# Optimization experiments

Measured on AMD Instinct MI355X. Metric: run time of the kernel, lower is better.

## Reference

```python
import jax, jax.numpy as jnp
import numpy as np

B_, S_, P_, D_ = 2, 512, 64, 1024
L_ = 4            # n_layer
DI_ = 2 * D_      # d_inner (expand=2)
DS_ = 16          # d_state
DC_ = 4           # d_conv
DR_ = D_ // 16    # dt_rank
PCD_ = 768        # prepend_cond_dim


def setup_inputs() -> dict:
    key = jax.random.key(0)
    ks = jax.random.split(key, 12)
    n = lambda k, s, sc=0.02: jax.random.normal(k, s, dtype=jnp.float32) * sc
    A_log = jnp.log(jnp.broadcast_to(jnp.arange(1, DS_ + 1, dtype=jnp.float32), (L_, DI_, DS_)))
    return {
        'x': jax.random.normal(ks[0], (B_, S_, D_), dtype=jnp.float32),
        'prepend_cond': jax.random.normal(ks[1], (B_, P_, PCD_), dtype=jnp.float32),
        'pre_w1': n(ks[2], (PCD_, D_)),
        'pre_w2': n(ks[3], (D_, D_)),
        'norm_w': jnp.ones((L_, D_), jnp.float32),
        'in_proj_w': n(ks[4], (L_, 2 * DI_, D_)),
        'conv_w': n(ks[5], (L_, DI_, DC_), 0.1),
        'conv_b': jnp.zeros((L_, DI_), jnp.float32),
        'x_proj_w': n(ks[6], (L_, DR_ + 2 * DS_, DI_)),
        'dt_proj_w': n(ks[7], (L_, DI_, DR_), 0.1),
        'dt_proj_b': jax.random.uniform(ks[8], (L_, DI_), jnp.float32, -4.0, -2.0),
        'A_log': A_log,
        'D_param': jnp.ones((L_, DI_), jnp.float32),
        'out_proj_w': n(ks[9], (L_, D_, DI_)),
        'final_norm_w': jnp.ones((D_,), jnp.float32),
    }


def rmsnorm(x, w, eps=1e-5):
    return x * jax.lax.rsqrt(jnp.mean(x * x, axis=-1, keepdims=True) + eps) * w


def mamba_block(x, ip_w, cw, cb, xp_w, dtp_w, dtp_b, A_log, Dp, op_w):
    B, S, _ = x.shape
    xz = jnp.einsum('bsd,ed->bse', x, ip_w)            # [B,S,2*DI]
    xi, z = jnp.split(xz, 2, axis=-1)
    # depthwise causal conv1d along time
    xt = xi.transpose(0, 2, 1)                          # [B,DI,S]
    conv = jax.lax.conv_general_dilated(
        xt, cw[:, None, :], (1,), [(DC_ - 1, 0)], feature_group_count=DI_) + cb[:, None]
    xi = jax.nn.silu(conv.transpose(0, 2, 1))           # [B,S,DI]
    xdbl = jnp.einsum('bse,fe->bsf', xi, xp_w)          # [B,S,DR+2*DS]
    dt, Bm, Cm = jnp.split(xdbl, [DR_, DR_ + DS_], axis=-1)
    dt = jax.nn.softplus(jnp.einsum('bsr,er->bse', dt, dtp_w) + dtp_b)  # [B,S,DI]
    A = -jnp.exp(A_log)                                 # [DI,DS]
    dA = jnp.exp(dt[..., None] * A)                     # [B,S,DI,DS]
    dBu = dt[..., None] * Bm[:, :, None, :] * xi[..., None]

    def step(h, t):
        da, dbu, c = t
        h = da * h + dbu                                # [B,DI,DS]
        return h, jnp.einsum('bes,bs->be', h, c)

    h0 = jnp.zeros((B, DI_, DS_), x.dtype)
    _, ys = jax.lax.scan(step, h0, (dA.transpose(1, 0, 2, 3), dBu.transpose(1, 0, 2, 3), Cm.transpose(1, 0, 2)))
    y = ys.transpose(1, 0, 2) + xi * Dp
    y = y * jax.nn.silu(z)
    return jnp.einsum('bse,de->bsd', y, op_w)


def reference(x, prepend_cond, pre_w1, pre_w2, norm_w, in_proj_w, conv_w, conv_b,
              x_proj_w, dt_proj_w, dt_proj_b, A_log, D_param, out_proj_w, final_norm_w):
    p = jax.nn.silu(prepend_cond @ pre_w1) @ pre_w2     # to_prepend_embed
    h = jnp.concatenate([p, x], axis=1)                 # [B, P+S, D]
    for l in range(L_):
        h = h + mamba_block(rmsnorm(h, norm_w[l]), in_proj_w[l], conv_w[l], conv_b[l],
                            x_proj_w[l], dt_proj_w[l], dt_proj_b[l], A_log[l],
                            D_param[l], out_proj_w[l])
    h = rmsnorm(h, final_norm_w)
    return h[:, P_:, :]
```

## Files before the change

kernel.cpp:

```cpp
#include <hip/hip_runtime.h>
#include <math.h>

#define B_ 2
#define S_ 512
#define P_ 64
#define T_ 576
#define D_ 1024
#define L_ 4
#define DI_ 2048
#define DS_ 16
#define DC_ 4
#define DR_ 64
#define PCD_ 768
#define M_ (B_*T_)
#define CCH 18
#define NC (T_/CCH)
#define XKS 16
#define OPK 4

typedef __attribute__((ext_vector_type(8))) short bf16x8;
typedef __attribute__((ext_vector_type(4))) float f32x4;

__device__ __forceinline__ float silu_f(float v) { return v / (1.f + __expf(-v)); }
__device__ __forceinline__ float softplus_f(float v) {
    return fmaxf(v, 0.f) + log1pf(__expf(-fabsf(v)));
}
__device__ __forceinline__ unsigned short bf16_rne(float x) {
    unsigned int b = __float_as_uint(x);
    b += 0x7fffu + ((b >> 16) & 1u);
    return (unsigned short)(b >> 16);
}
__device__ __forceinline__ float bf16_to_f(unsigned short u) {
    return __uint_as_float((unsigned int)u << 16);
}

typedef const void __attribute__((address_space(1)))* gas_t;
typedef void __attribute__((address_space(3)))* las_t;
__device__ __forceinline__ void async16(const void* g, void* l) {
    __builtin_amdgcn_global_load_lds((gas_t)g, (las_t)l, 16, 0, 0);
}

template<int EPI, int BN>
__global__ __launch_bounds__(256) void gemm_mfma_kernel(
    const unsigned short* __restrict__ A, const unsigned short* __restrict__ W,
    float* __restrict__ C, float* __restrict__ C2,
    int M, int N, int K, int Kchunk)
{
    constexpr int NF = BN / 32;
    __shared__ unsigned short As[128 * 32];
    __shared__ unsigned short Bs[BN * 32];
    const int tid = threadIdx.x;
    const int wave = tid >> 6;
    const int lane = tid & 63;
    const int m0 = blockIdx.y * 128, n0 = blockIdx.x * BN;
    const int kbase = blockIdx.z * Kchunk;
    const int wm = (wave >> 1) * 64, wn = (wave & 1) * (BN / 2);

    const int srow = (wave << 5) + (lane >> 2);
    const int selem = (lane & 3) * 8;
    const unsigned short* gA = A + (size_t)(m0 + srow) * K + kbase + selem;
    const unsigned short* gB = W + (size_t)(n0 + srow) * K + kbase + selem;
    unsigned short* lA = As + (wave << 5) * 32;
    unsigned short* lB = Bs + (wave << 5) * 32;

    f32x4 acc[4][NF];
    #pragma unroll
    for (int i = 0; i < 4; ++i)
        #pragma unroll
        for (int j = 0; j < NF; ++j)
            acc[i][j] = (f32x4){0.f, 0.f, 0.f, 0.f};

    const int fr = lane & 15;
    const int fq = lane >> 4;
    const int aoff = (wm + fr) * 32 + fq * 8;
    const int boff = (wn + fr) * 32 + fq * 8;

    for (int k0 = 0; k0 < Kchunk; k0 += 32) {
        async16(gA, lA);
        async16(gA + (size_t)16 * K, lA + 16 * 32);
        if (BN == 128 || wave < BN / 32) {
            async16(gB, lB);
            async16(gB + (size_t)16 * K, lB + 16 * 32);
        }
        gA += 32; gB += 32;
        __syncthreads();
        bf16x8 af[4], bf[NF];
        #pragma unroll
        for (int i = 0; i < 4; ++i) af[i] = *(const bf16x8*)&As[aoff + i * 512];
        #pragma unroll
        for (int j = 0; j < NF; ++j) bf[j] = *(const bf16x8*)&Bs[boff + j * 512];
        #pragma unroll
        for (int i = 0; i < 4; ++i)
            #pragma unroll
            for (int j = 0; j < NF; ++j)
                acc[i][j] = __builtin_amdgcn_mfma_f32_16x16x32_bf16(
                    af[i], bf[j], acc[i][j], 0, 0, 0);
        __syncthreads();
    }

    #pragma unroll
    for (int i = 0; i < 4; ++i) {
        const int m = m0 + wm + i * 16 + fq * 4;
        #pragma unroll
        for (int j = 0; j < NF; ++j) {
            const int n = n0 + wn + j * 16 + fr;
            if (EPI == 6) {
                float* p = C + ((size_t)blockIdx.z * M + m) * N + n;
                #pragma unroll
                for (int r = 0; r < 4; ++r)
                    p[(size_t)r * N] = acc[i][j][r];
            } else if (EPI == 7) {
                if (n < DI_) {
                    unsigned short* p = (unsigned short*)C + (size_t)m * DI_ + n;
                    #pragma unroll
                    for (int r = 0; r < 4; ++r)
                        p[(size_t)r * DI_] = bf16_rne(acc[i][j][r]);
                } else {
                    unsigned short* p = (unsigned short*)C2 + (size_t)m * DI_ + (n - DI_);
                    #pragma unroll
                    for (int r = 0; r < 4; ++r)
                        p[(size_t)r * DI_] = bf16_rne(silu_f(acc[i][j][r]));
                }
            }
        }
    }
}

__global__ __launch_bounds__(256) void dtproj_kernel(
    const unsigned short* __restrict__ dtr,
    const unsigned short* __restrict__ Wb,
    const float* __restrict__ bias,
    float* __restrict__ dtb)
{
    __shared__ float As[16][DR_];
    const int tid = threadIdx.x;
    const int e = blockIdx.x * 256 + tid;
    const int m0 = blockIdx.y * 16;
    {
        const ushort4 a4 = ((const ushort4*)(dtr + (size_t)m0 * DR_))[tid];
        float* dst = &As[0][0] + tid * 4;
        dst[0] = bf16_to_f(a4.x);
        dst[1] = bf16_to_f(a4.y);
        dst[2] = bf16_to_f(a4.z);
        dst[3] = bf16_to_f(a4.w);
    }
    float w[DR_];
    {
        const ushort4* wp = (const ushort4*)(Wb + (size_t)e * DR_);
        #pragma unroll
        for (int q = 0; q < 16; ++q) {
            const ushort4 v = wp[q];
            w[q * 4 + 0] = bf16_to_f(v.x);
            w[q * 4 + 1] = bf16_to_f(v.y);
            w[q * 4 + 2] = bf16_to_f(v.z);
            w[q * 4 + 3] = bf16_to_f(v.w);
        }
    }
    __syncthreads();
    const float bb = bias[e];
    #pragma unroll
    for (int m = 0; m < 16; ++m) {
        float acc = 0.f;
        #pragma unroll
        for (int r = 0; r < DR_; ++r) acc = fmaf(As[m][r], w[r], acc);
        dtb[(size_t)(m0 + m) * DI_ + e] = softplus_f(acc + bb);
    }
}

__global__ __launch_bounds__(256) void xproj_mfma_kernel(
    const unsigned short* __restrict__ A,
    const unsigned short* __restrict__ W,
    float* __restrict__ P)
{
    __shared__ unsigned short As[128 * 32];
    __shared__ unsigned short Bs[96 * 32];
    const int tid = threadIdx.x;
    const int wave = tid >> 6;
    const int lane = tid & 63;
    const int m0 = blockIdx.y * 128;
    const int kbase = blockIdx.x * (DI_ / XKS);
    const int wm = (wave >> 1) * 64, wn = (wave & 1) * 48;

    const int srow = (wave << 5) + (lane >> 2);
    const int selem = (lane & 3) * 8;
    const unsigned short* gA = A + (size_t)(m0 + srow) * DI_ + kbase + selem;
    const unsigned short* gB = W + (size_t)srow * DI_ + kbase + selem;
    unsigned short* lA = As + (wave << 5) * 32;
    unsigned short* lB = Bs + (wave << 5) * 32;

    f32x4 acc[4][3];
    #pragma unroll
    for (int i = 0; i < 4; ++i)
        #pragma unroll
        for (int j = 0; j < 3; ++j)
            acc[i][j] = (f32x4){0.f, 0.f, 0.f, 0.f};

    const int fr = lane & 15;
    const int fq = lane >> 4;
    const int aoff = (wm + fr) * 32 + fq * 8;
    const int boff = (wn + fr) * 32 + fq * 8;

    #pragma unroll
    for (int kk = 0; kk < 4; ++kk) {
        async16(gA, lA);
        async16(gA + (size_t)16 * DI_, lA + 16 * 32);
        if (wave < 3) {
            async16(gB, lB);
            async16(gB + (size_t)16 * DI_, lB + 16 * 32);
        }
        gA += 32; gB += 32;
        __syncthreads();
        bf16x8 af[4], bf[3];
        #pragma unroll
        for (int i = 0; i < 4; ++i) af[i] = *(const bf16x8*)&As[aoff + i * 512];
        #pragma unroll
        for (int j = 0; j < 3; ++j) bf[j] = *(const bf16x8*)&Bs[boff + j * 512];
        #pragma unroll
        for (int i = 0; i < 4; ++i)
            #pragma unroll
            for (int j = 0; j < 3; ++j)
                acc[i][j] = __builtin_amdgcn_mfma_f32_16x16x32_bf16(
                    af[i], bf[j], acc[i][j], 0, 0, 0);
        __syncthreads();
    }

    float* Pb = P + ((size_t)blockIdx.x * M_ + m0) * 96;
    #pragma unroll
    for (int i = 0; i < 4; ++i) {
        const int m = wm + i * 16 + fq * 4;
        #pragma unroll
        for (int j = 0; j < 3; ++j) {
            const int n = wn + j * 16 + fr;
            #pragma unroll
            for (int r = 0; r < 4; ++r)
                Pb[(size_t)(m + r) * 96 + n] = acc[i][j][r];
        }
    }
}

__global__ __launch_bounds__(256) void xproj_reduce_kernel(
    const float* __restrict__ P, float* __restrict__ Bc, float* __restrict__ Cc,
    unsigned short* __restrict__ dtr_bf)
{
    const int i = blockIdx.x * 256 + threadIdx.x;
    if (i >= M_ * 96) return;
    float s = 0.f;
    #pragma unroll
    for (int ks = 0; ks < XKS; ++ks) s += P[(size_t)ks * (M_ * 96) + i];
    const int m = i / 96;
    const int n = i - m * 96;
    if (n < DR_)            dtr_bf[(size_t)m * DR_ + n] = bf16_rne(s);
    else if (n < DR_ + DS_) Bc[(size_t)m * DS_ + (n - DR_)] = s;
    else                    Cc[(size_t)m * DS_ + (n - DR_ - DS_)] = s;
}

__global__ __launch_bounds__(256) void cvt_bf16_kernel(
    const float* __restrict__ in, unsigned short* __restrict__ out, int n4)
{
    const int i = blockIdx.x * 256 + threadIdx.x;
    if (i >= n4) return;
    const float4 v = ((const float4*)in)[i];
    ushort4 o;
    o.x = bf16_rne(v.x); o.y = bf16_rne(v.y);
    o.z = bf16_rne(v.z); o.w = bf16_rne(v.w);
    ((ushort4*)out)[i] = o;
}

__global__ __launch_bounds__(256) void cvt4_kernel(
    const float* __restrict__ s0, unsigned short* __restrict__ d0, int n0,
    const float* __restrict__ s1, unsigned short* __restrict__ d1, int n1,
    const float* __restrict__ s2, unsigned short* __restrict__ d2, int n2,
    const float* __restrict__ s3, unsigned short* __restrict__ d3, int n3)
{
    const int i = blockIdx.x * 256 + threadIdx.x;
    const float* s; unsigned short* d; int off;
    if (i < n0)                { s = s0; d = d0; off = i; }
    else if (i < n0 + n1)      { s = s1; d = d1; off = i - n0; }
    else if (i < n0 + n1 + n2) { s = s2; d = d2; off = i - n0 - n1; }
    else if (i < n0 + n1 + n2 + n3) { s = s3; d = d3; off = i - n0 - n1 - n2; }
    else return;
    const float4 v = ((const float4*)s)[off];
    ushort4 o;
    o.x = bf16_rne(v.x); o.y = bf16_rne(v.y);
    o.z = bf16_rne(v.z); o.w = bf16_rne(v.w);
    ((ushort4*)d)[off] = o;
}

__global__ __launch_bounds__(256) void cvt_transpose_kernel(
    const float* __restrict__ in, unsigned short* __restrict__ out, int K, int N)
{
    __shared__ float t[64][65];
    const int k0 = blockIdx.x * 64;
    const int n0 = blockIdx.y * 64;
    const int tx = threadIdx.x & 63;
    const int ty = threadIdx.x >> 6;
    #pragma unroll
    for (int j = 0; j < 16; ++j) {
        const int kk = ty * 16 + j;
        t[kk][tx] = in[(size_t)(k0 + kk) * N + n0 + tx];
    }
    __syncthreads();
    #pragma unroll
    for (int j = 0; j < 16; ++j) {
        const int nn = ty * 16 + j;
        out[(size_t)(n0 + nn) * K + k0 + tx] = bf16_rne(t[tx][nn]);
    }
}

__global__ __launch_bounds__(256) void reduce_silu_bf16_kernel(
    const float* __restrict__ P, unsigned short* __restrict__ o, int MN, int ns)
{
    const int i = blockIdx.x * 256 + threadIdx.x;
    if (i >= MN) return;
    float s = 0.f;
    for (int k = 0; k < ns; ++k) s += P[(size_t)k * MN + i];
    o[i] = bf16_rne(silu_f(s));
}
__global__ __launch_bounds__(256) void reduce_fp32_kernel(
    const float* __restrict__ P, float* __restrict__ o, int MN, int ns)
{
    const int i = blockIdx.x * 256 + threadIdx.x;
    if (i >= MN) return;
    float s = 0.f;
    for (int k = 0; k < ns; ++k) s += P[(size_t)k * MN + i];
    o[i] = s;
}

__global__ __launch_bounds__(256) void outproj_rmsnorm_kernel(
    const float* __restrict__ P, float* __restrict__ h,
    const float* __restrict__ w, unsigned short* __restrict__ outb, int donorm)
{
    const int r = blockIdx.x;
    const int i = r * 256 + threadIdx.x;
    float4 v = ((float4*)h)[i];
    #pragma unroll
    for (int k = 0; k < OPK; ++k) {
        const float4 a4 = ((const float4*)P)[i + k * (M_ * D_ / 4)];
        v.x += a4.x; v.y += a4.y; v.z += a4.z; v.w += a4.w;
    }
    ((float4*)h)[i] = v;
    if (!donorm) return;
    float ss = v.x * v.x + v.y * v.y + v.z * v.z + v.w * v.w;
    ss += __shfl_xor(ss, 32, 64);
    ss += __shfl_xor(ss, 16, 64);
    ss += __shfl_xor(ss, 8, 64);
    ss += __shfl_xor(ss, 4, 64);
    ss += __shfl_xor(ss, 2, 64);
    ss += __shfl_xor(ss, 1, 64);
    __shared__ float red[4];
    if ((threadIdx.x & 63) == 0) red[threadIdx.x >> 6] = ss;
    __syncthreads();
    const float tot = red[0] + red[1] + red[2] + red[3];
    const float scale = rsqrtf(tot * (1.f / D_) + 1e-5f);
    const float4 wv = ((const float4*)w)[threadIdx.x];
    ushort4 o;
    o.x = bf16_rne(v.x * scale * wv.x);
    o.y = bf16_rne(v.y * scale * wv.y);
    o.z = bf16_rne(v.z * scale * wv.z);
    o.w = bf16_rne(v.w * scale * wv.w);
    ((ushort4*)(outb + (size_t)r * D_))[threadIdx.x] = o;
}

__global__ __launch_bounds__(256) void assemble_h_kernel(
    const float* __restrict__ p, const float* __restrict__ x, float* __restrict__ h)
{
    const int idx = blockIdx.x * 256 + threadIdx.x;
    const int r = idx >> 8;
    const int c = idx & 255;
    const int b = r / T_;
    const int t = r - b * T_;
    float4 v;
    if (t < P_) v = ((const float4*)p)[(size_t)(b * P_ + t) * 256 + c];
    else        v = ((const float4*)x)[(size_t)(b * S_ + (t - P_)) * 256 + c];
    ((float4*)h)[idx] = v;
}

__global__ __launch_bounds__(256) void rmsnorm_bf16_kernel(
    const float* __restrict__ x, const float* __restrict__ w,
    unsigned short* __restrict__ outb)
{
    const int r = blockIdx.x;
    const float4 v = ((const float4*)(x + (size_t)r * D_))[threadIdx.x];
    float ss = v.x * v.x + v.y * v.y + v.z * v.z + v.w * v.w;
    ss += __shfl_xor(ss, 32, 64);
    ss += __shfl_xor(ss, 16, 64);
    ss += __shfl_xor(ss, 8, 64);
    ss += __shfl_xor(ss, 4, 64);
    ss += __shfl_xor(ss, 2, 64);
    ss += __shfl_xor(ss, 1, 64);
    __shared__ float red[4];
    if ((threadIdx.x & 63) == 0) red[threadIdx.x >> 6] = ss;
    __syncthreads();
    const float tot = red[0] + red[1] + red[2] + red[3];
    const float scale = rsqrtf(tot * (1.f / D_) + 1e-5f);
    const float4 wv = ((const float4*)w)[threadIdx.x];
    ushort4 o;
    o.x = bf16_rne(v.x * scale * wv.x);
    o.y = bf16_rne(v.y * scale * wv.y);
    o.z = bf16_rne(v.z * scale * wv.z);
    o.w = bf16_rne(v.w * scale * wv.w);
    ((ushort4*)(outb + (size_t)r * D_))[threadIdx.x] = o;
}

__global__ __launch_bounds__(256) void final_rmsnorm_kernel(
    const float* __restrict__ h, const float* __restrict__ w, float* __restrict__ out)
{
    const int r = blockIdx.x;
    const int b = r / S_;
    const int s = r - b * S_;
    const int hr = b * T_ + P_ + s;
    const float4 v = ((const float4*)(h + (size_t)hr * D_))[threadIdx.x];
    float ss = v.x * v.x + v.y * v.y + v.z * v.z + v.w * v.w;
    ss += __shfl_xor(ss, 32, 64);
    ss += __shfl_xor(ss, 16, 64);
    ss += __shfl_xor(ss, 8, 64);
    ss += __shfl_xor(ss, 4, 64);
    ss += __shfl_xor(ss, 2, 64);
    ss += __shfl_xor(ss, 1, 64);
    __shared__ float red[4];
    if ((threadIdx.x & 63) == 0) red[threadIdx.x >> 6] = ss;
    __syncthreads();
    const float tot = red[0] + red[1] + red[2] + red[3];
    const float scale = rsqrtf(tot * (1.f / D_) + 1e-5f);
    const float4 wv = ((const float4*)w)[threadIdx.x];
    float4 o;
    o.x = v.x * scale * wv.x; o.y = v.y * scale * wv.y;
    o.z = v.z * scale * wv.z; o.w = v.w * scale * wv.w;
    ((float4*)(out + (size_t)r * D_))[threadIdx.x] = o;
}

__global__ __launch_bounds__(256) void conv_silu_kernel(
    const unsigned short* __restrict__ xb, const float* __restrict__ cw,
    const float* __restrict__ cb, unsigned short* __restrict__ xib)
{
    __shared__ float xs[67][64];
    const int tid = threadIdx.x;
    const int tx = tid & 63;
    const int ty = tid >> 6;
    const int r0 = blockIdx.x * 64;
    const int e0 = blockIdx.y * 64;
    const int bt0 = (r0 / T_) * T_;

    for (int j = ty; j < 67; j += 4) {
        const int r = r0 + j - 3;
        xs[j][tx] = (r >= bt0) ? bf16_to_f(xb[(size_t)r * DI_ + e0 + tx]) : 0.f;
    }
    __syncthreads();
    const float4 w = *(const float4*)(cw + (size_t)(e0 + tx) * 4);
    const float bias = cb[e0 + tx];
    #pragma unroll
    for (int j = 0; j < 16; ++j) {
        const int rl = ty * 16 + j;
        float v = bias;
        v = fmaf(w.x, xs[rl + 0][tx], v);
        v = fmaf(w.y, xs[rl + 1][tx], v);
        v = fmaf(w.z, xs[rl + 2][tx], v);
        v = fmaf(w.w, xs[rl + 3][tx], v);
        xib[(size_t)(r0 + rl) * DI_ + e0 + tx] = bf16_rne(silu_f(v));
    }
}

__global__ __launch_bounds__(256) void scan_chunk1_kernel(
    const float* __restrict__ dtm,
    const float* __restrict__ Bc,
    const unsigned short* __restrict__ xib,
    const float* __restrict__ A_log,
    float* __restrict__ Ap, float* __restrict__ Hp)
{
    __shared__ float4 Bs[CCH][4];
    const int tid = threadIdx.x;
    const int e = ((blockIdx.x & 7) << 8) + tid;
    const int cb = blockIdx.x >> 3;
    const int b = cb & (B_ - 1);
    const int c = cb >> 1;
    const int r0 = b * T_ + c * CCH;
    for (int i = tid; i < CCH * DS_; i += 256)
        ((float*)Bs)[i] = Bc[(size_t)r0 * DS_ + i];
    float A2[DS_], h[DS_], a[DS_];
    const float* Ae = A_log + (size_t)e * DS_;
    #pragma unroll
    for (int s = 0; s < DS_; ++s) {
        A2[s] = -__expf(Ae[s]) * 1.44269504f;
        h[s] = 0.f; a[s] = 1.f;
    }
    __syncthreads();
    const float* dp = dtm + (size_t)r0 * DI_ + e;
    const unsigned short* up = xib + (size_t)r0 * DI_ + e;
    #pragma unroll
    for (int t = 0; t < CCH; ++t) {
        const float dtv = dp[(size_t)t * DI_];
        const float dtu = dtv * bf16_to_f(up[(size_t)t * DI_]);
        #pragma unroll
        for (int q = 0; q < 4; ++q) {
            const float4 bq = Bs[t][q];
            const float* bb = &bq.x;
            #pragma unroll
            for (int j = 0; j < 4; ++j) {
                const int s = q * 4 + j;
                const float da = __builtin_amdgcn_exp2f(dtv * A2[s]);
                a[s] *= da;
                h[s] = fmaf(da, h[s], bb[j] * dtu);
            }
        }
    }
    const size_t o = (size_t)cb * DS_ * DI_ + e;
    #pragma unroll
    for (int s = 0; s < DS_; ++s) {
        Ap[o + (size_t)s * DI_] = a[s];
        Hp[o + (size_t)s * DI_] = h[s];
    }
}

__global__ __launch_bounds__(256) void scan_chunk2_kernel(
    float* __restrict__ Ap, float* __restrict__ Hp)
{
    const int g = blockIdx.x * 256 + threadIdx.x;
    float h = 0.f;
    #pragma unroll
    for (int c = 0; c < NC; ++c) {
        const size_t o = (size_t)c * (B_ * DI_ * DS_) + g;
        const float ap = Ap[o];
        const float hp = Hp[o];
        Hp[o] = h;
        h = fmaf(ap, h, hp);
    }
}

__global__ __launch_bounds__(256) void scan_chunk3_kernel(
    const float* __restrict__ dtm,
    const float* __restrict__ Bc,
    const float* __restrict__ Cc,
    const unsigned short* __restrict__ xib,
    const unsigned short* __restrict__ szb,
    const float* __restrict__ A_log, const float* __restrict__ Dp,
    const float* __restrict__ Hin, unsigned short* __restrict__ y)
{
    __shared__ float4 Bs[CCH][4], Cs[CCH][4];
    const int tid = threadIdx.x;
    const int e = ((blockIdx.x & 7) << 8) + tid;
    const int cb = blockIdx.x >> 3;
    const int b = cb & (B_ - 1);
    const int c = cb >> 1;
    const int r0 = b * T_ + c * CCH;
    for (int i = tid; i < CCH * DS_; i += 256) {
        ((float*)Bs)[i] = Bc[(size_t)r0 * DS_ + i];
        ((float*)Cs)[i] = Cc[(size_t)r0 * DS_ + i];
    }
    float A2[DS_], h[DS_];
    const float* Ae = A_log + (size_t)e * DS_;
    const float dpe = Dp[e];
    const size_t ho = (size_t)cb * DS_ * DI_ + e;
    #pragma unroll
    for (int s = 0; s < DS_; ++s) {
        A2[s] = -__expf(Ae[s]) * 1.44269504f;
        h[s] = Hin[ho + (size_t)s * DI_];
    }
    __syncthreads();
    const float* dp = dtm + (size_t)r0 * DI_ + e;
    const unsigned short* up = xib + (size_t)r0 * DI_ + e;
    const unsigned short* sp = szb + (size_t)r0 * DI_ + e;
    unsigned short* yp = y + (size_t)r0 * DI_ + e;
    #pragma unroll
    for (int t = 0; t < CCH; ++t) {
        const float dtv = dp[(size_t)t * DI_];
        const float u   = bf16_to_f(up[(size_t)t * DI_]);
        const float dtu = dtv * u;
        float y0 = 0.f, y1 = 0.f, y2 = 0.f, y3 = 0.f;
        #pragma unroll
        for (int q = 0; q < 4; ++q) {
            const float4 bq = Bs[t][q];
            const float4 cq = Cs[t][q];
            const float* bb = &bq.x;
            const float* cc = &cq.x;
            #pragma unroll
            for (int j = 0; j < 4; ++j) {
                const int s = q * 4 + j;
                const float da = __builtin_amdgcn_exp2f(dtv * A2[s]);
                h[s] = fmaf(da, h[s], bb[j] * dtu);
                if (j == 0)      y0 = fmaf(h[s], cc[j], y0);
                else if (j == 1) y1 = fmaf(h[s], cc[j], y1);
                else if (j == 2) y2 = fmaf(h[s], cc[j], y2);
                else             y3 = fmaf(h[s], cc[j], y3);
            }
        }
        const float ysum = (y0 + y1) + (y2 + y3);
        const float yv = fmaf(u, dpe, ysum) * bf16_to_f(sp[(size_t)t * DI_]);
        yp[(size_t)t * DI_] = bf16_rne(yv);
    }
}

extern "C" void kernel_launch(void* const* d_in, const int* in_sizes, int n_in,
                              void* d_out, int out_size, void* d_ws, size_t ws_size,
                              hipStream_t stream)
{
    const float* x       = (const float*)d_in[0];
    const float* pc      = (const float*)d_in[1];
    const float* pre_w1  = (const float*)d_in[2];
    const float* pre_w2  = (const float*)d_in[3];
    const float* norm_w  = (const float*)d_in[4];
    const float* ip_w    = (const float*)d_in[5];
    const float* conv_w  = (const float*)d_in[6];
    const float* conv_b  = (const float*)d_in[7];
    const float* xp_w    = (const float*)d_in[8];
    const float* dtp_w   = (const float*)d_in[9];
    const float* dtp_b   = (const float*)d_in[10];
    const float* A_log   = (const float*)d_in[11];
    const float* D_param = (const float*)d_in[12];
    const float* op_w    = (const float*)d_in[13];
    const float* fnw     = (const float*)d_in[14];
    float* out = (float*)d_out;

    float* ws = (float*)d_ws;
    float* h    = ws;  ws += (size_t)M_ * D_;
    float* xz   = ws;  ws += (size_t)M_ * 2 * DI_;
    float* dtb  = ws;  ws += (size_t)M_ * DI_;
    float* Pbuf = ws;  ws += (size_t)XKS * M_ * 96;
    float* Bc   = ws;  ws += (size_t)DS_ * M_;
    float* Cc   = ws;  ws += (size_t)DS_ * M_;
    unsigned short* xn_bf  = (unsigned short*)ws;  ws += (size_t)M_ * D_ / 2;
    unsigned short* yb_bf  = (unsigned short*)ws;  ws += (size_t)M_ * DI_ / 2;
    unsigned short* xi_bf  = (unsigned short*)ws;  ws += (size_t)M_ * DI_ / 2;
    unsigned short* xb_bf  = (unsigned short*)ws;  ws += (size_t)M_ * DI_ / 2;
    unsigned short* szb_bf = (unsigned short*)ws;  ws += (size_t)M_ * DI_ / 2;
    unsigned short* dtr_bf = (unsigned short*)ws;  ws += (size_t)M_ * DR_ / 2;
    unsigned short* wbuf   = (unsigned short*)ws;  ws += (size_t)2 * DI_ * D_ / 2;
    unsigned short* xpw_bf = (unsigned short*)ws;  ws += (size_t)96 * DI_ / 2;
    unsigned short* dtpw_bf= (unsigned short*)ws;  ws += (size_t)DI_ * DR_ / 2;
    unsigned short* opw_bf = (unsigned short*)ws;  ws += (size_t)D_ * DI_ / 2;

    float* Ap = xz;
    float* Hp = xz + (size_t)NC * B_ * DI_ * DS_;

    unsigned short* pc_bf   = xi_bf;
    unsigned short* w1t_bf  = wbuf;
    unsigned short* w2t_bf  = wbuf + (size_t)D_ * PCD_;
    unsigned short* tmp1_bf = xn_bf;
    float*          tmp2    = Pbuf;
    float*          P2buf   = dtb;
    float*          Pop     = xz;

    const dim3 blk(256);

    cvt_bf16_kernel<<<dim3(B_ * P_ * PCD_ / 4 / 256), blk, 0, stream>>>(
        pc, pc_bf, B_ * P_ * PCD_ / 4);
    cvt_transpose_kernel<<<dim3(PCD_ / 64, D_ / 64), blk, 0, stream>>>(
        pre_w1, w1t_bf, PCD_, D_);
    cvt_transpose_kernel<<<dim3(D_ / 64, D_ / 64), blk, 0, stream>>>(
        pre_w2, w2t_bf, D_, D_);
    gemm_mfma_kernel<6, 64><<<dim3(D_ / 64, 1, 12), blk, 0, stream>>>(
        pc_bf, w1t_bf, Pbuf, nullptr, B_ * P_, D_, PCD_, PCD_ / 12);
    reduce_silu_bf16_kernel<<<dim3(B_ * P_ * D_ / 256), blk, 0, stream>>>(
        Pbuf, tmp1_bf, B_ * P_ * D_, 12);
    gemm_mfma_kernel<6, 64><<<dim3(D_ / 64, 1, 16), blk, 0, stream>>>(
        tmp1_bf, w2t_bf, P2buf, nullptr, B_ * P_, D_, D_, D_ / 16);
    reduce_fp32_kernel<<<dim3(B_ * P_ * D_ / 256), blk, 0, stream>>>(
        P2buf, tmp2, B_ * P_ * D_, 16);
    assemble_h_kernel<<<dim3(M_ * D_ / 4 / 256), blk, 0, stream>>>(tmp2, x, h);

    const int n_ip  = 2 * DI_ * D_ / 4;
    const int n_xp  = 96 * DI_ / 4;
    const int n_dtp = DI_ * DR_ / 4;
    const int n_op  = D_ * DI_ / 4;

    rmsnorm_bf16_kernel<<<dim3(M_), blk, 0, stream>>>(h, norm_w, xn_bf);

    for (int l = 0; l < L_; ++l) {
        cvt4_kernel<<<dim3((n_ip + n_xp + n_dtp + n_op + 255) / 256), blk, 0, stream>>>(
            ip_w + (size_t)l * 2 * DI_ * D_, wbuf, n_ip,
            xp_w + (size_t)l * 96 * DI_, xpw_bf, n_xp,
            dtp_w + (size_t)l * DI_ * DR_, dtpw_bf, n_dtp,
            op_w + (size_t)l * D_ * DI_, opw_bf, n_op);
        gemm_mfma_kernel<7, 64><<<dim3(2 * DI_ / 64, M_ / 128, 1), blk, 0, stream>>>(
            xn_bf, wbuf, (float*)xb_bf, (float*)szb_bf, M_, 2 * DI_, D_, D_);
        conv_silu_kernel<<<dim3(M_ / 64, DI_ / 64), blk, 0, stream>>>(
            xb_bf, conv_w + (size_t)l * DI_ * DC_, conv_b + (size_t)l * DI_,
            xi_bf);
        xproj_mfma_kernel<<<dim3(XKS, M_ / 128), blk, 0, stream>>>(
            xi_bf, xpw_bf, Pbuf);
        xproj_reduce_kernel<<<dim3((M_ * 96 + 255) / 256), blk, 0, stream>>>(
            Pbuf, Bc, Cc, dtr_bf);
        dtproj_kernel<<<dim3(DI_ / 256, M_ / 16), blk, 0, stream>>>(
            dtr_bf, dtpw_bf, dtp_b + (size_t)l * DI_, dtb);
        scan_chunk1_kernel<<<dim3(NC * B_ * DI_ / 256), blk, 0, stream>>>(
            dtb, Bc, xi_bf, A_log + (size_t)l * DI_ * DS_, Ap, Hp);
        scan_chunk2_kernel<<<dim3(B_ * DI_ * DS_ / 256), blk, 0, stream>>>(Ap, Hp);
        scan_chunk3_kernel<<<dim3(NC * B_ * DI_ / 256), blk, 0, stream>>>(
            dtb, Bc, Cc, xi_bf, szb_bf, A_log + (size_t)l * DI_ * DS_,
            D_param + (size_t)l * DI_, Hp, yb_bf);
        gemm_mfma_kernel<6, 64><<<dim3(D_ / 64, M_ / 128, OPK), blk, 0, stream>>>(
            yb_bf, opw_bf, Pop, nullptr, M_, D_, DI_, DI_ / OPK);
        outproj_rmsnorm_kernel<<<dim3(M_), blk, 0, stream>>>(
            Pop, h, norm_w + (size_t)((l + 1) & 3) * D_, xn_bf, l < L_ - 1);
    }

    final_rmsnorm_kernel<<<dim3(B_ * S_), blk, 0, stream>>>(h, fnw, out);
}
```

Before: 681.1 us.

## Fuse dt projection into scan kernels, double-buffer weight conversion, bf16 out-proj partials

Removes the standalone dtproj kernel and its fp32 dt buffer, recomputing dt (a 64-wide dot plus softplus) inside both scan_chunk1 and scan_chunk3 from dtr held in LDS. The per-layer weight conversion is folded into the rmsnorm and outproj-residual kernels as extra blocks that convert the next layer's weights into a second buffer set. Out-proj split-K partials are now stored as bf16 instead of fp32, halving that traffic at some precision cost. The dt projection is now computed twice per layer, and each scan thread must hold 64 weight values in registers.

```diff
diff --git a/kernel.cpp b/kernel.cpp
--- a/kernel.cpp
+++ b/kernel.cpp
@@ -18,6 +18,13 @@
 #define XKS 16
 #define OPK 4
 
+#define N_IP (2*DI_*D_/4)
+#define N_XP (96*DI_/4)
+#define N_DTP (DI_*DR_/4)
+#define N_OP (D_*DI_/4)
+#define CVB ((N_IP + N_XP + N_DTP + N_OP + 255) / 256)
+#define SETSZ ((size_t)2*DI_*D_ + 96*DI_ + DI_*DR_ + D_*DI_)
+
 typedef __attribute__((ext_vector_type(8))) short bf16x8;
 typedef __attribute__((ext_vector_type(4))) float f32x4;
 
@@ -38,6 +45,25 @@
 typedef void __attribute__((address_space(3)))* las_t;
 __device__ __forceinline__ void async16(const void* g, void* l) {
     __builtin_amdgcn_global_load_lds((gas_t)g, (las_t)l, 16, 0, 0);
+}
+
+__device__ __forceinline__ void cvt4_body(int i,
+    const float* s0, unsigned short* d0, int n0,
+    const float* s1, unsigned short* d1, int n1,
+    const float* s2, unsigned short* d2, int n2,
+    const float* s3, unsigned short* d3, int n3)
+{
+    const float* s; unsigned short* d; int off;
+    if (i < n0)                     { s = s0; d = d0; off = i; }
+    else if (i < n0 + n1)           { s = s1; d = d1; off = i - n0; }
+    else if (i < n0 + n1 + n2)      { s = s2; d = d2; off = i - n0 - n1; }
+    else if (i < n0 + n1 + n2 + n3) { s = s3; d = d3; off = i - n0 - n1 - n2; }
+    else return;
+    const float4 v = ((const float4*)s)[off];
+    ushort4 o;
+    o.x = bf16_rne(v.x); o.y = bf16_rne(v.y);
+    o.z = bf16_rne(v.z); o.w = bf16_rne(v.w);
+    ((ushort4*)d)[off] = o;
 }
 
 template<int EPI, int BN>
@@ -109,6 +135,12 @@
                 #pragma unroll
                 for (int r = 0; r < 4; ++r)
                     p[(size_t)r * N] = acc[i][j][r];
+            } else if (EPI == 8) {
+                unsigned short* p = (unsigned short*)C +
+                                    ((size_t)blockIdx.z * M + m) * N + n;
+                #pragma unroll
+                for (int r = 0; r < 4; ++r)
+                    p[(size_t)r * N] = bf16_rne(acc[i][j][r]);
             } else if (EPI == 7) {
                 if (n < DI_) {
                     unsigned short* p = (unsigned short*)C + (size_t)m * DI_ + n;
@@ -126,47 +158,6 @@
     }
 }
 
-__global__ __launch_bounds__(256) void dtproj_kernel(
-    const unsigned short* __restrict__ dtr,
-    const unsigned short* __restrict__ Wb,
-    const float* __restrict__ bias,
-    float* __restrict__ dtb)
-{
-    __shared__ float As[16][DR_];
-    const int tid = threadIdx.x;
-    const int e = blockIdx.x * 256 + tid;
-    const int m0 = blockIdx.y * 16;
-    {
-        const ushort4 a4 = ((const ushort4*)(dtr + (size_t)m0 * DR_))[tid];
-        float* dst = &As[0][0] + tid * 4;
-        dst[0] = bf16_to_f(a4.x);
-        dst[1] = bf16_to_f(a4.y);
-        dst[2] = bf16_to_f(a4.z);
-        dst[3] = bf16_to_f(a4.w);
-    }
-    float w[DR_];
-    {
-        const ushort4* wp = (const ushort4*)(Wb + (size_t)e * DR_);
-        #pragma unroll
-        for (int q = 0; q < 16; ++q) {
-            const ushort4 v = wp[q];
-            w[q * 4 + 0] = bf16_to_f(v.x);
-            w[q * 4 + 1] = bf16_to_f(v.y);
-            w[q * 4 + 2] = bf16_to_f(v.z);
-            w[q * 4 + 3] = bf16_to_f(v.w);
-        }
-    }
-    __syncthreads();
-    const float bb = bias[e];
-    #pragma unroll
-    for (int m = 0; m < 16; ++m) {
-        float acc = 0.f;
-        #pragma unroll
-        for (int r = 0; r < DR_; ++r) acc = fmaf(As[m][r], w[r], acc);
-        dtb[(size_t)(m0 + m) * DI_ + e] = softplus_f(acc + bb);
-    }
-}
-
 __global__ __launch_bounds__(256) void xproj_mfma_kernel(
     const unsigned short* __restrict__ A,
     const unsigned short* __restrict__ W,
@@ -266,26 +257,6 @@
     ((ushort4*)out)[i] = o;
 }
 
-__global__ __launch_bounds__(256) void cvt4_kernel(
-    const float* __restrict__ s0, unsigned short* __restrict__ d0, int n0,
-    const float* __restrict__ s1, unsigned short* __restrict__ d1, int n1,
-    const float* __restrict__ s2, unsigned short* __restrict__ d2, int n2,
-    const float* __restrict__ s3, unsigned short* __restrict__ d3, int n3)
-{
-    const int i = blockIdx.x * 256 + threadIdx.x;
-    const float* s; unsigned short* d; int off;
-    if (i < n0)                { s = s0; d = d0; off = i; }
-    else if (i < n0 + n1)      { s = s1; d = d1; off = i - n0; }
-    else if (i < n0 + n1 + n2) { s = s2; d = d2; off = i - n0 - n1; }
-    else if (i < n0 + n1 + n2 + n3) { s = s3; d = d3; off = i - n0 - n1 - n2; }
-    else return;
-    const float4 v = ((const float4*)s)[off];
-    ushort4 o;
-    o.x = bf16_rne(v.x); o.y = bf16_rne(v.y);
-    o.z = bf16_rne(v.z); o.w = bf16_rne(v.w);
-    ((ushort4*)d)[off] = o;
-}
-
 __global__ __launch_bounds__(256) void cvt_transpose_kernel(
     const float* __restrict__ in, unsigned short* __restrict__ out, int K, int N)
 {
@@ -326,17 +297,28 @@
     o[i] = s;
 }
 
-__global__ __launch_bounds__(256) void outproj_rmsnorm_kernel(
-    const float* __restrict__ P, float* __restrict__ h,
-    const float* __restrict__ w, unsigned short* __restrict__ outb, int donorm)
-{
-    const int r = blockIdx.x;
+__global__ __launch_bounds__(256) void outproj_rmsnorm_cvt_kernel(
+    const unsigned short* __restrict__ P, float* __restrict__ h,
+    const float* __restrict__ w, unsigned short* __restrict__ outb, int donorm,
+    const float* s0, unsigned short* d0, int n0,
+    const float* s1, unsigned short* d1, int n1,
+    const float* s2, unsigned short* d2, int n2,
+    const float* s3, unsigned short* d3, int n3)
+{
+    const int bid = blockIdx.x;
+    if (bid >= M_) {
+        cvt4_body((bid - M_) * 256 + threadIdx.x,
+                  s0, d0, n0, s1, d1, n1, s2, d2, n2, s3, d3, n3);
+        return;
+    }
+    const int r = bid;
     const int i = r * 256 + threadIdx.x;
     float4 v = ((float4*)h)[i];
     #pragma unroll
     for (int k = 0; k < OPK; ++k) {
-        const float4 a4 = ((const float4*)P)[i + k * (M_ * D_ / 4)];
-        v.x += a4.x; v.y += a4.y; v.z += a4.z; v.w += a4.w;
+        const ushort4 a4 = ((const ushort4*)P)[(size_t)k * (M_ * D_ / 4) + i];
+        v.x += bf16_to_f(a4.x); v.y += bf16_to_f(a4.y);
+        v.z += bf16_to_f(a4.z); v.w += bf16_to_f(a4.w);
     }
     ((float4*)h)[i] = v;
     if (!donorm) return;
@@ -375,11 +357,21 @@
     ((float4*)h)[idx] = v;
 }
 
-__global__ __launch_bounds__(256) void rmsnorm_bf16_kernel(
+__global__ __launch_bounds__(256) void rmsnorm_cvt_kernel(
     const float* __restrict__ x, const float* __restrict__ w,
-    unsigned short* __restrict__ outb)
-{
-    const int r = blockIdx.x;
+    unsigned short* __restrict__ outb,
+    const float* s0, unsigned short* d0, int n0,
+    const float* s1, unsigned short* d1, int n1,
+    const float* s2, unsigned short* d2, int n2,
+    const float* s3, unsigned short* d3, int n3)
+{
+    const int bid = blockIdx.x;
+    if (bid >= M_) {
+        cvt4_body((bid - M_) * 256 + threadIdx.x,
+                  s0, d0, n0, s1, d1, n1, s2, d2, n2, s3, d3, n3);
+        return;
+    }
+    const int r = bid;
     const float4 v = ((const float4*)(x + (size_t)r * D_))[threadIdx.x];
     float ss = v.x * v.x + v.y * v.y + v.z * v.z + v.w * v.w;
     ss += __shfl_xor(ss, 32, 64);
@@ -461,13 +453,16 @@
 }
 
 __global__ __launch_bounds__(256) void scan_chunk1_kernel(
-    const float* __restrict__ dtm,
+    const unsigned short* __restrict__ dtr,
+    const unsigned short* __restrict__ dtw,
+    const float* __restrict__ dtbias,
     const float* __restrict__ Bc,
     const unsigned short* __restrict__ xib,
     const float* __restrict__ A_log,
     float* __restrict__ Ap, float* __restrict__ Hp)
 {
     __shared__ float4 Bs[CCH][4];
+    __shared__ float dtrs[CCH][DR_];
     const int tid = threadIdx.x;
     const int e = ((blockIdx.x & 7) << 8) + tid;
     const int cb = blockIdx.x >> 3;
@@ -476,6 +471,12 @@
     const int r0 = b * T_ + c * CCH;
     for (int i = tid; i < CCH * DS_; i += 256)
         ((float*)Bs)[i] = Bc[(size_t)r0 * DS_ + i];
+    for (int i = tid; i < CCH * DR_ / 4; i += 256) {
+        const ushort4 v4 = ((const ushort4*)(dtr + (size_t)r0 * DR_))[i];
+        float* d = &dtrs[0][0] + i * 4;
+        d[0] = bf16_to_f(v4.x); d[1] = bf16_to_f(v4.y);
+        d[2] = bf16_to_f(v4.z); d[3] = bf16_to_f(v4.w);
+    }
     float A2[DS_], h[DS_], a[DS_];
     const float* Ae = A_log + (size_t)e * DS_;
     #pragma unroll
@@ -484,11 +485,31 @@
         h[s] = 0.f; a[s] = 1.f;
     }
     __syncthreads();
-    const float* dp = dtm + (size_t)r0 * DI_ + e;
+    float dt[CCH];
+    {
+        float w[DR_];
+        const ushort4* wp = (const ushort4*)(dtw + (size_t)e * DR_);
+        #pragma unroll
+        for (int q = 0; q < 16; ++q) {
+            const ushort4 v = wp[q];
+            w[q * 4 + 0] = bf16_to_f(v.x);
+            w[q * 4 + 1] = bf16_to_f(v.y);
+            w[q * 4 + 2] = bf16_to_f(v.z);
+            w[q * 4 + 3] = bf16_to_f(v.w);
+        }
+        const float bb = dtbias[e];
+        #pragma unroll
+        for (int t = 0; t < CCH; ++t) {
+            float acc = 0.f;
+            #pragma unroll
+            for (int r = 0; r < DR_; ++r) acc = fmaf(dtrs[t][r], w[r], acc);
+            dt[t] = softplus_f(acc + bb);
+        }
+    }
     const unsigned short* up = xib + (size_t)r0 * DI_ + e;
     #pragma unroll
     for (int t = 0; t < CCH; ++t) {
-        const float dtv = dp[(size_t)t * DI_];
+        const float dtv = dt[t];
         const float dtu = dtv * bf16_to_f(up[(size_t)t * DI_]);
         #pragma unroll
         for (int q = 0; q < 4; ++q) {
@@ -527,7 +548,9 @@
 }
 
 __global__ __launch_bounds__(256) void scan_chunk3_kernel(
-    const float* __restrict__ dtm,
+    const unsigned short* __restrict__ dtr,
+    const unsigned short* __restrict__ dtw,
+    const float* __restrict__ dtbias,
     const float* __restrict__ Bc,
     const float* __restrict__ Cc,
     const unsigned short* __restrict__ xib,
@@ -536,6 +559,7 @@
     const float* __restrict__ Hin, unsigned short* __restrict__ y)
 {
     __shared__ float4 Bs[CCH][4], Cs[CCH][4];
+    __shared__ float dtrs[CCH][DR_];
     const int tid = threadIdx.x;
     const int e = ((blockIdx.x & 7) << 8) + tid;
     const int cb = blockIdx.x >> 3;
@@ -546,6 +570,12 @@
         ((float*)Bs)[i] = Bc[(size_t)r0 * DS_ + i];
         ((float*)Cs)[i] = Cc[(size_t)r0 * DS_ + i];
     }
+    for (int i = tid; i < CCH * DR_ / 4; i += 256) {
+        const ushort4 v4 = ((const ushort4*)(dtr + (size_t)r0 * DR_))[i];
+        float* d = &dtrs[0][0] + i * 4;
+        d[0] = bf16_to_f(v4.x); d[1] = bf16_to_f(v4.y);
+        d[2] = bf16_to_f(v4.z); d[3] = bf16_to_f(v4.w);
+    }
     float A2[DS_], h[DS_];
     const float* Ae = A_log + (size_t)e * DS_;
     const float dpe = Dp[e];
@@ -556,13 +586,33 @@
         h[s] = Hin[ho + (size_t)s * DI_];
     }
     __syncthreads();
-    const float* dp = dtm + (size_t)r0 * DI_ + e;
+    float dt[CCH];
+    {
+        float w[DR_];
+        const ushort4* wp = (const ushort4*)(dtw + (size_t)e * DR_);
+        #pragma unroll
+        for (int q = 0; q < 16; ++q) {
+            const ushort4 v = wp[q];
+            w[q * 4 + 0] = bf16_to_f(v.x);
+            w[q * 4 + 1] = bf16_to_f(v.y);
+            w[q * 4 + 2] = bf16_to_f(v.z);
+            w[q * 4 + 3] = bf16_to_f(v.w);
+        }
+        const float bb = dtbias[e];
+        #pragma unroll
+        for (int t = 0; t < CCH; ++t) {
+            float acc = 0.f;
+            #pragma unroll
+            for (int r = 0; r < DR_; ++r) acc = fmaf(dtrs[t][r], w[r], acc);
+            dt[t] = softplus_f(acc + bb);
+        }
+    }
     const unsigned short* up = xib + (size_t)r0 * DI_ + e;
     const unsigned short* sp = szb + (size_t)r0 * DI_ + e;
     unsigned short* yp = y + (size_t)r0 * DI_ + e;
     #pragma unroll
     for (int t = 0; t < CCH; ++t) {
-        const float dtv = dp[(size_t)t * DI_];
+        const float dtv = dt[t];
         const float u   = bf16_to_f(up[(size_t)t * DI_]);
         const float dtu = dtv * u;
         float y0 = 0.f, y1 = 0.f, y2 = 0.f, y3 = 0.f;
@@ -613,7 +663,7 @@
     float* ws = (float*)d_ws;
     float* h    = ws;  ws += (size_t)M_ * D_;
     float* xz   = ws;  ws += (size_t)M_ * 2 * DI_;
-    float* dtb  = ws;  ws += (size_t)M_ * DI_;
+    float* scr  = ws;  ws += (size_t)M_ * DI_;
     float* Pbuf = ws;  ws += (size_t)XKS * M_ * 96;
     float* Bc   = ws;  ws += (size_t)DS_ * M_;
     float* Cc   = ws;  ws += (size_t)DS_ * M_;
@@ -623,21 +673,28 @@
     unsigned short* xb_bf  = (unsigned short*)ws;  ws += (size_t)M_ * DI_ / 2;
     unsigned short* szb_bf = (unsigned short*)ws;  ws += (size_t)M_ * DI_ / 2;
     unsigned short* dtr_bf = (unsigned short*)ws;  ws += (size_t)M_ * DR_ / 2;
-    unsigned short* wbuf   = (unsigned short*)ws;  ws += (size_t)2 * DI_ * D_ / 2;
-    unsigned short* xpw_bf = (unsigned short*)ws;  ws += (size_t)96 * DI_ / 2;
-    unsigned short* dtpw_bf= (unsigned short*)ws;  ws += (size_t)DI_ * DR_ / 2;
-    unsigned short* opw_bf = (unsigned short*)ws;  ws += (size_t)D_ * DI_ / 2;
+    unsigned short* wsets  = (unsigned short*)ws;  ws += SETSZ;
+    ws += SETSZ;
+
+    unsigned short* ipw_b[2], *xpw_b[2], *dtpw_b[2], *opw_b[2];
+    for (int s = 0; s < 2; ++s) {
+        unsigned short* base = wsets + (size_t)s * SETSZ;
+        ipw_b[s]  = base;
+        xpw_b[s]  = base + (size_t)2 * DI_ * D_;
+        dtpw_b[s] = xpw_b[s] + (size_t)96 * DI_;
+        opw_b[s]  = dtpw_b[s] + (size_t)DI_ * DR_;
+    }
 
     float* Ap = xz;
     float* Hp = xz + (size_t)NC * B_ * DI_ * DS_;
 
     unsigned short* pc_bf   = xi_bf;
-    unsigned short* w1t_bf  = wbuf;
-    unsigned short* w2t_bf  = wbuf + (size_t)D_ * PCD_;
+    unsigned short* w1t_bf  = ipw_b[0];
+    unsigned short* w2t_bf  = ipw_b[0] + (size_t)D_ * PCD_;
     unsigned short* tmp1_bf = xn_bf;
     float*          tmp2    = Pbuf;
-    float*          P2buf   = dtb;
-    float*          Pop     = xz;
+    float*          P2buf   = scr;
+    unsigned short* Pop     = (unsigned short*)xz;
 
     const dim3 blk(256);
 
@@ -657,40 +714,40 @@
         P2buf, tmp2, B_ * P_ * D_, 16);
     assemble_h_kernel<<<dim3(M_ * D_ / 4 / 256), blk, 0, stream>>>(tmp2, x, h);
 
-    const int n_ip  = 2 * DI_ * D_ / 4;
-    const int n_xp  = 96 * DI_ / 4;
-    const int n_dtp = DI_ * DR_ / 4;
-    const int n_op  = D_ * DI_ / 4;
-
-    rmsnorm_bf16_kernel<<<dim3(M_), blk, 0, stream>>>(h, norm_w, xn_bf);
+    rmsnorm_cvt_kernel<<<dim3(M_ + CVB), blk, 0, stream>>>(
+        h, norm_w, xn_bf,
+        ip_w, ipw_b[0], N_IP,
+        xp_w, xpw_b[0], N_XP,
+        dtp_w, dtpw_b[0], N_DTP,
+        op_w, opw_b[0], N_OP);
 
     for (int l = 0; l < L_; ++l) {
-        cvt4_kernel<<<dim3((n_ip + n_xp + n_dtp + n_op + 255) / 256), blk, 0, stream>>>(
-            ip_w + (size_t)l * 2 * DI_ * D_, wbuf, n_ip,
-            xp_w + (size_t)l * 96 * DI_, xpw_bf, n_xp,
-            dtp_w + (size_t)l * DI_ * DR_, dtpw_bf, n_dtp,
-            op_w + (size_t)l * D_ * DI_, opw_bf, n_op);
+        const int s = l & 1;
         gemm_mfma_kernel<7, 64><<<dim3(2 * DI_ / 64, M_ / 128, 1), blk, 0, stream>>>(
-            xn_bf, wbuf, (float*)xb_bf, (float*)szb_bf, M_, 2 * DI_, D_, D_);
+            xn_bf, ipw_b[s], (float*)xb_bf, (float*)szb_bf, M_, 2 * DI_, D_, D_);
         conv_silu_kernel<<<dim3(M_ / 64, DI_ / 64), blk, 0, stream>>>(
             xb_bf, conv_w + (size_t)l * DI_ * DC_, conv_b + (size_t)l * DI_,
             xi_bf);
         xproj_mfma_kernel<<<dim3(XKS, M_ / 128), blk, 0, stream>>>(
-            xi_bf, xpw_bf, Pbuf);
+            xi_bf, xpw_b[s], Pbuf);
         xproj_reduce_kernel<<<dim3((M_ * 96 + 255) / 256), blk, 0, stream>>>(
             Pbuf, Bc, Cc, dtr_bf);
-        dtproj_kernel<<<dim3(DI_ / 256, M_ / 16), blk, 0, stream>>>(
-            dtr_bf, dtpw_bf, dtp_b + (size_t)l * DI_, dtb);
         scan_chunk1_kernel<<<dim3(NC * B_ * DI_ / 256), blk, 0, stream>>>(
-            dtb, Bc, xi_bf, A_log + (size_t)l * DI_ * DS_, Ap, Hp);
+            dtr_bf, dtpw_b[s], dtp_b + (size_t)l * DI_, Bc, xi_bf,
+            A_log + (size_t)l * DI_ * DS_, Ap, Hp);
         scan_chunk2_kernel<<<dim3(B_ * DI_ * DS_ / 256), blk, 0, stream>>>(Ap, Hp);
         scan_chunk3_kernel<<<dim3(NC * B_ * DI_ / 256), blk, 0, stream>>>(
-            dtb, Bc, Cc, xi_bf, szb_bf, A_log + (size_t)l * DI_ * DS_,
-            D_param + (size_t)l * DI_, Hp, yb_bf);
-        gemm_mfma_kernel<6, 64><<<dim3(D_ / 64, M_ / 128, OPK), blk, 0, stream>>>(
-            yb_bf, opw_bf, Pop, nullptr, M_, D_, DI_, DI_ / OPK);
-        outproj_rmsnorm_kernel<<<dim3(M_), blk, 0, stream>>>(
-            Pop, h, norm_w + (size_t)((l + 1) & 3) * D_, xn_bf, l < L_ - 1);
+            dtr_bf, dtpw_b[s], dtp_b + (size_t)l * DI_, Bc, Cc, xi_bf, szb_bf,
+            A_log + (size_t)l * DI_ * DS_, D_param + (size_t)l * DI_, Hp, yb_bf);
+        gemm_mfma_kernel<8, 64><<<dim3(D_ / 64, M_ / 128, OPK), blk, 0, stream>>>(
+            yb_bf, opw_b[s], (float*)Pop, nullptr, M_, D_, DI_, DI_ / OPK);
+        const int docvt = (l + 1 < L_);
+        outproj_rmsnorm_cvt_kernel<<<dim3(M_ + (docvt ? CVB : 0)), blk, 0, stream>>>(
+            Pop, h, norm_w + (size_t)((l + 1) & 3) * D_, xn_bf, l < L_ - 1,
+            ip_w + (size_t)(l + 1) * 2 * DI_ * D_, ipw_b[s ^ 1], docvt ? N_IP : 0,
+            xp_w + (size_t)(l + 1) * 96 * DI_, xpw_b[s ^ 1], docvt ? N_XP : 0,
+            dtp_w + (size_t)(l + 1) * DI_ * DR_, dtpw_b[s ^ 1], docvt ? N_DTP : 0,
+            op_w + (size_t)(l + 1) * D_ * DI_, opw_b[s ^ 1], docvt ? N_OP : 0);
     }
 
     final_rmsnorm_kernel<<<dim3(B_ * S_), blk, 0, stream>>>(h, fnw, out);
```

After: 673.9 us. About the same (-1.1%).
